# Kernel tuning notes

Hardware: AMD Instinct MI355X
Metric: run time of the kernel (lower is better)

The kernel has to match this reference:

```python
import jax, jax.numpy as jnp
import numpy as np

# BEV grid parameters from calculate_birds_eye_view_parameters([-50,50,0.5],[-50,50,0.5],[-10,10,20])
BEV_RES = np.array([0.5, 0.5, 20.0], dtype=np.float32)
BEV_START = np.array([-49.75, -49.75, 0.0], dtype=np.float32)   # lower + res/2
BEV_DIM = (200, 200, 1)                                          # (X, Y, Z)

B, N, D, H, W, C = 2, 6, 48, 28, 60, 64


def setup_inputs() -> dict:
    key = jax.random.key(0)
    k1, k2, k3 = jax.random.split(key, 3)
    x = jax.random.normal(k1, (B, N, D, H, W, C), dtype=jnp.float32)
    geo_xy = jax.random.uniform(k2, (B, N, D, H, W, 2), minval=-55.0, maxval=55.0)
    geo_z = jax.random.uniform(k3, (B, N, D, H, W, 1), minval=-12.0, maxval=12.0)
    geometry = jnp.concatenate([geo_xy, geo_z], axis=-1).astype(jnp.float32)
    return {"x": x, "geometry": geometry}


def reference(x, geometry):
    # x:        [B, N, D, H, W, C] camera frustum features
    # geometry: [B, N, D, H, W, 3] ego-frame (x, y, z) of each frustum point
    b, n, d, h, w, c = x.shape
    res = jnp.asarray(BEV_RES)
    start = jnp.asarray(BEV_START)
    dim = jnp.asarray(BEV_DIM, dtype=jnp.int32)
    X, Y, Z = BEV_DIM
    nvox = X * Y * Z

    # voxel index; torch .long() truncates toward zero -> astype(int32) matches
    vox = ((geometry - (start - res / 2.0)) / res).astype(jnp.int32)   # [B,N,D,H,W,3]
    vox = vox.reshape(b, -1, 3)                                        # [B, Np, 3]
    feat = x.reshape(b, -1, c)                                         # [B, Np, C]

    valid = jnp.all((vox >= 0) & (vox < dim), axis=-1)                 # [B, Np]
    ranks = vox[..., 0] * (Y * Z) + vox[..., 1] * Z + vox[..., 2]      # [B, Np]
    seg = jnp.where(valid, ranks + jnp.arange(b, dtype=jnp.int32)[:, None] * nvox,
                    b * nvox)                                          # invalid -> dump segment

    # per-voxel sum == sorted cumsum + dedup-diff of VoxelsSumming
    pooled = jax.ops.segment_sum(feat.reshape(-1, c), seg.reshape(-1),
                                 num_segments=b * nvox + 1)            # [B*nvox+1, C]
    bev = pooled[: b * nvox].reshape(b, X, Y, Z, c)                    # [B, X, Y, Z, C]
    # torch scatters into [Z, X, Y, C], permutes to [Z, C, X, Y], squeezes Z=1 -> [B, C, X, Y]
    out = bev.transpose(0, 3, 4, 1, 2).reshape(b, Z * c, X, Y)
    return out
```

## Files before the change

kernel.cpp:

```cpp
#include <hip/hip_runtime.h>

#define Bq 2
#define Nn 6
#define Dd 48
#define Hh 28
#define Ww 60
#define Cc 64
#define Xd 200
#define Yd 200
#define NP (Nn*Dd*Hh*Ww)
#define TOTP (Bq*NP)
#define NVOX (Xd*Yd)
#define NSEG (Bq*NVOX)
#define NB1  79

__global__ __launch_bounds__(1024) void zero_cnt(int* __restrict__ cnt)
{
    int i = blockIdx.x * 1024 + threadIdx.x;
    if (i < NSEG) cnt[i] = 0;
}

__global__ __launch_bounds__(256) void phase_a(
    const float* __restrict__ geom, int* __restrict__ rank, int* __restrict__ cnt)
{
    int p = blockIdx.x * 256 + threadIdx.x;
    if (p >= TOTP) return;
    float gx = geom[(long)p*3 + 0];
    float gy = geom[(long)p*3 + 1];
    float gz = geom[(long)p*3 + 2];
    int vx = (int)((gx + 50.0f) / 0.5f);
    int vy = (int)((gy + 50.0f) / 0.5f);
    int vz = (int)((gz + 10.0f) / 20.0f);
    int seg = -1;
    if (vx >= 0 && vx < Xd && vy >= 0 && vy < Yd && vz == 0) {
        int b = (p >= NP) ? 1 : 0;
        seg = b * NVOX + vx * Yd + vy;
        atomicAdd(&cnt[seg], 1);
    }
    rank[p] = seg;
}

__global__ __launch_bounds__(1024) void scan_p1(
    const int* __restrict__ cnt, int* __restrict__ start, int* __restrict__ bsum)
{
    __shared__ int sh[1024];
    int tid = threadIdx.x;
    int i = blockIdx.x * 1024 + tid;
    int v = (i < NSEG) ? cnt[i] : 0;
    sh[tid] = v;
    __syncthreads();
    for (int off = 1; off < 1024; off <<= 1) {
        int t = (tid >= off) ? sh[tid - off] : 0;
        __syncthreads();
        sh[tid] += t;
        __syncthreads();
    }
    if (i < NSEG) start[i] = sh[tid] - v;
    if (tid == 1023) bsum[blockIdx.x] = sh[1023];
}

__global__ __launch_bounds__(128) void scan_p2(int* __restrict__ bsum)
{
    __shared__ int sh[128];
    int tid = threadIdx.x;
    int v = (tid < NB1) ? bsum[tid] : 0;
    sh[tid] = v;
    __syncthreads();
    for (int off = 1; off < 128; off <<= 1) {
        int t = (tid >= off) ? sh[tid - off] : 0;
        __syncthreads();
        sh[tid] += t;
        __syncthreads();
    }
    if (tid < NB1) bsum[tid] = sh[tid] - v;
}

__global__ __launch_bounds__(1024) void scan_p3(
    int* __restrict__ start, const int* __restrict__ bsum)
{
    int i = blockIdx.x * 1024 + threadIdx.x;
    if (i < NSEG) start[i] += bsum[blockIdx.x];
}

__global__ __launch_bounds__(256) void phase_c(
    const int* __restrict__ rank, int* __restrict__ start, int* __restrict__ order)
{
    int p = blockIdx.x * 256 + threadIdx.x;
    if (p >= TOTP) return;
    int seg = rank[p];
    if (seg < 0) return;
    int pos = atomicAdd(&start[seg], 1);
    order[pos] = p;
}

__global__ __launch_bounds__(256) void phase_d(
    const int* __restrict__ endp, const int* __restrict__ order,
    const float* __restrict__ x, float* __restrict__ out)
{
    __shared__ float tile[32][68];
    int blk  = blockIdx.x;
    int b    = blk / (NVOX/32);
    int xy0  = (blk % (NVOX/32)) * 32;
    int wv   = threadIdx.x >> 6;
    int lane = threadIdx.x & 63;
    int seg0 = b * NVOX + xy0 + wv * 8;

    int e = 0;
    if (lane < 9) {
        int idx = seg0 - 1 + lane;
        e = (idx >= 0) ? endp[idx] : 0;
    }

    int g = lane >> 4;
    int q = (lane & 15) * 4;

    for (int v = 0; v < 8; ++v) {
        int begin = __shfl(e, v);
        int endv  = __shfl(e, v + 1);
        float4 sum = make_float4(0.f, 0.f, 0.f, 0.f);
        int t = begin + g;
        for (; t + 4 < endv; t += 8) {
            int p0 = order[t];
            int p1 = order[t + 4];
            const float4 a0 = *(const float4*)(x + (long)p0 * Cc + q);
            const float4 a1 = *(const float4*)(x + (long)p1 * Cc + q);
            sum.x += a0.x + a1.x; sum.y += a0.y + a1.y;
            sum.z += a0.z + a1.z; sum.w += a0.w + a1.w;
        }
        if (t < endv) {
            int p0 = order[t];
            const float4 a0 = *(const float4*)(x + (long)p0 * Cc + q);
            sum.x += a0.x; sum.y += a0.y; sum.z += a0.z; sum.w += a0.w;
        }
        #pragma unroll
        for (int m = 16; m <= 32; m <<= 1) {
            sum.x += __shfl_xor(sum.x, m);
            sum.y += __shfl_xor(sum.y, m);
            sum.z += __shfl_xor(sum.z, m);
            sum.w += __shfl_xor(sum.w, m);
        }
        if (g == 0) *(float4*)&tile[wv*8 + v][q] = sum;
    }
    __syncthreads();

    float* dst = out + (long)b * Cc * NVOX + xy0;
    int xy = threadIdx.x & 31;
    int c0 = threadIdx.x >> 5;
    #pragma unroll
    for (int s = 0; s < 8; ++s) {
        int c = s * 8 + c0;
        dst[(long)c * NVOX + xy] = tile[xy][c];
    }
}

__global__ __launch_bounds__(256) void fiery_scatter_direct(
    const float* __restrict__ x, const float* __restrict__ geom,
    float* __restrict__ out)
{
    int wid  = blockIdx.x * 4 + (threadIdx.x >> 6);
    int lane = threadIdx.x & 63;
    if (wid >= TOTP) return;
    long gb = (long)wid * 3;
    float gx = geom[gb+0], gy = geom[gb+1], gz = geom[gb+2];
    int vx = (int)((gx + 50.0f) / 0.5f);
    int vy = (int)((gy + 50.0f) / 0.5f);
    int vz = (int)((gz + 10.0f) / 20.0f);
    if (!(vx >= 0 && vx < Xd && vy >= 0 && vy < Yd && vz == 0)) return;
    int b = (wid >= NP) ? 1 : 0;
    float vv = x[(long)wid * Cc + lane];
    long dst = ((long)(b * Cc + lane)) * NVOX + (vx * Yd + vy);
    atomicAdd(&out[dst], vv);
}

extern "C" void kernel_launch(void* const* d_in, const int* in_sizes, int n_in,
                              void* d_out, int out_size, void* d_ws, size_t ws_size,
                              hipStream_t stream)
{
    const float* x    = (const float*)d_in[0];
    const float* geom = (const float*)d_in[1];
    float* out = (float*)d_out;

    size_t need = ((size_t)TOTP * 2 + (size_t)NSEG * 2 + 128) * sizeof(int);
    if (ws_size >= need) {
        int* rank  = (int*)d_ws;
        int* order = rank  + TOTP;
        int* cnt   = order + TOTP;
        int* start = cnt   + NSEG;
        int* bsum  = start + NSEG;

        zero_cnt<<<NB1, 1024, 0, stream>>>(cnt);
        phase_a<<<TOTP/256, 256, 0, stream>>>(geom, rank, cnt);
        scan_p1<<<NB1, 1024, 0, stream>>>(cnt, start, bsum);
        scan_p2<<<1, 128, 0, stream>>>(bsum);
        scan_p3<<<NB1, 1024, 0, stream>>>(start, bsum);
        phase_c<<<TOTP/256, 256, 0, stream>>>(rank, start, order);
        phase_d<<<Bq*(NVOX/32), 256, 0, stream>>>(start, order, x, out);
    } else {
        hipMemsetAsync(out, 0, (size_t)out_size * sizeof(float), stream);
        fiery_scatter_direct<<<TOTP/4, 256, 0, stream>>>(x, geom, out);
    }
}
```

Baseline: 130.3 us.

## Flatten per-wave voxel gather with LDS-staged indices and shared atomics

Each wave in the gather kernel now processes all points of its 8 voxels as one flat list instead of looping voxel by voxel. It first stages the point indices, tagged with their local voxel id, in shared memory, then gathers feature rows and accumulates them into the output tile with shared-memory float atomics. This is meant to remove lane idling and per-voxel shuffle reductions when voxels hold only a few points. It adds LDS atomic contention and a barrier inside a wave-divergent branch. A fallback to the per-voxel loop remains for waves whose 8 voxels hold more than 512 points.

```diff
diff --git a/kernel.cpp b/kernel.cpp
--- a/kernel.cpp
+++ b/kernel.cpp
@@ -13,6 +13,7 @@
 #define NVOX (Xd*Yd)
 #define NSEG (Bq*NVOX)
 #define NB1  79
+#define CAP  512
 
 __global__ __launch_bounds__(1024) void zero_cnt(int* __restrict__ cnt)
 {
@@ -97,6 +98,7 @@
     const int* __restrict__ endp, const int* __restrict__ order,
     const float* __restrict__ x, float* __restrict__ out)
 {
+    __shared__ int   ord_sh[4][CAP];
     __shared__ float tile[32][68];
     int blk  = blockIdx.x;
     int b    = blk / (NVOX/32);
@@ -110,36 +112,64 @@
         int idx = seg0 - 1 + lane;
         e = (idx >= 0) ? endp[idx] : 0;
     }
+    int eb0 = __shfl(e,0), eb1 = __shfl(e,1), eb2 = __shfl(e,2),
+        eb3 = __shfl(e,3), eb4 = __shfl(e,4), eb5 = __shfl(e,5),
+        eb6 = __shfl(e,6), eb7 = __shfl(e,7), eb8 = __shfl(e,8);
+    int count = eb8 - eb0;
+
+    {
+        int r = wv*8 + (lane >> 3);
+        int c = (lane & 7) * 8;
+        float4 z = make_float4(0.f, 0.f, 0.f, 0.f);
+        *(float4*)&tile[r][c]     = z;
+        *(float4*)&tile[r][c + 4] = z;
+    }
 
     int g = lane >> 4;
     int q = (lane & 15) * 4;
 
-    for (int v = 0; v < 8; ++v) {
-        int begin = __shfl(e, v);
-        int endv  = __shfl(e, v + 1);
-        float4 sum = make_float4(0.f, 0.f, 0.f, 0.f);
-        int t = begin + g;
-        for (; t + 4 < endv; t += 8) {
-            int p0 = order[t];
-            int p1 = order[t + 4];
-            const float4 a0 = *(const float4*)(x + (long)p0 * Cc + q);
-            const float4 a1 = *(const float4*)(x + (long)p1 * Cc + q);
-            sum.x += a0.x + a1.x; sum.y += a0.y + a1.y;
-            sum.z += a0.z + a1.z; sum.w += a0.w + a1.w;
+    if (count <= CAP) {
+        for (int i = lane; i < count; i += 64) {
+            int gi  = eb0 + i;
+            int pid = order[gi];
+            int v = (gi >= eb1) + (gi >= eb2) + (gi >= eb3) + (gi >= eb4)
+                  + (gi >= eb5) + (gi >= eb6) + (gi >= eb7);
+            ord_sh[wv][i] = pid | (v << 24);
         }
-        if (t < endv) {
-            int p0 = order[t];
-            const float4 a0 = *(const float4*)(x + (long)p0 * Cc + q);
-            sum.x += a0.x; sum.y += a0.y; sum.z += a0.z; sum.w += a0.w;
+        __syncthreads();
+
+        #pragma unroll 4
+        for (int i = g; i < count; i += 4) {
+            int w   = ord_sh[wv][i];
+            int pid = w & 0xFFFFFF;
+            int v   = w >> 24;
+            const float4 a = *(const float4*)(x + (long)pid * Cc + q);
+            float* row = &tile[wv*8 + v][q];
+            atomicAdd(&row[0], a.x);
+            atomicAdd(&row[1], a.y);
+            atomicAdd(&row[2], a.z);
+            atomicAdd(&row[3], a.w);
         }
-        #pragma unroll
-        for (int m = 16; m <= 32; m <<= 1) {
-            sum.x += __shfl_xor(sum.x, m);
-            sum.y += __shfl_xor(sum.y, m);
-            sum.z += __shfl_xor(sum.z, m);
-            sum.w += __shfl_xor(sum.w, m);
+    } else {
+        __syncthreads();
+        for (int v = 0; v < 8; ++v) {
+            int begin = __shfl(e, v);
+            int endv  = __shfl(e, v + 1);
+            float4 sum = make_float4(0.f, 0.f, 0.f, 0.f);
+            for (int t = begin + g; t < endv; t += 4) {
+                int p0 = order[t];
+                const float4 a0 = *(const float4*)(x + (long)p0 * Cc + q);
+                sum.x += a0.x; sum.y += a0.y; sum.z += a0.z; sum.w += a0.w;
+            }
+            #pragma unroll
+            for (int m = 16; m <= 32; m <<= 1) {
+                sum.x += __shfl_xor(sum.x, m);
+                sum.y += __shfl_xor(sum.y, m);
+                sum.z += __shfl_xor(sum.z, m);
+                sum.w += __shfl_xor(sum.w, m);
+            }
+            if (g == 0) *(float4*)&tile[wv*8 + v][q] = sum;
         }
-        if (g == 0) *(float4*)&tile[wv*8 + v][q] = sum;
     }
     __syncthreads();
 
```

After: 362.2 us. 178% more time.

## Stage gathered feature rows into LDS via async global_load_lds in pooling kernel

Applied to the files above, without the earlier changes.

The pooling kernel now stages each wave's point indices in shared memory. It then issues up to 32 row gathers per round with global_load_lds, waits on them once, and accumulates the eight voxel sums from LDS instead of chaining dependent global loads per voxel. The goal is more memory-level parallelism across all eight voxels a wave owns. In exchange it uses a large amount of LDS (about 41 KB per block), which lowers occupancy, and it adds a full vmcnt wait per round. Waves with more than 512 points fall back to a direct gather path.

```diff
diff --git a/kernel.cpp b/kernel.cpp
--- a/kernel.cpp
+++ b/kernel.cpp
@@ -13,6 +13,8 @@
 #define NVOX (Xd*Yd)
 #define NSEG (Bq*NVOX)
 #define NB1  79
+#define CAP  512
+#define RND  32
 
 __global__ __launch_bounds__(1024) void zero_cnt(int* __restrict__ cnt)
 {
@@ -93,10 +95,17 @@
     order[pos] = p;
 }
 
+#define DMA_ROW(gp, lp) \
+    __builtin_amdgcn_global_load_lds( \
+        (const __attribute__((address_space(1))) void*)(gp), \
+        (__attribute__((address_space(3))) void*)(lp), 4, 0, 0)
+
 __global__ __launch_bounds__(256) void phase_d(
     const int* __restrict__ endp, const int* __restrict__ order,
     const float* __restrict__ x, float* __restrict__ out)
 {
+    __shared__ int   ord_sh[4][CAP];
+    __shared__ float pbuf[4][RND][Cc];
     __shared__ float tile[32][68];
     int blk  = blockIdx.x;
     int b    = blk / (NVOX/32);
@@ -110,36 +119,72 @@
         int idx = seg0 - 1 + lane;
         e = (idx >= 0) ? endp[idx] : 0;
     }
+    int eb0 = __shfl(e, 0);
+    int rb[9];
+    #pragma unroll
+    for (int j = 0; j < 9; ++j) rb[j] = __shfl(e, j) - eb0;
+    int count = rb[8];
 
     int g = lane >> 4;
     int q = (lane & 15) * 4;
 
+    float4 A[8];
+    #pragma unroll
+    for (int v = 0; v < 8; ++v) A[v] = make_float4(0.f, 0.f, 0.f, 0.f);
+
+    if (count <= CAP) {
+        for (int i = lane; i < count; i += 64)
+            ord_sh[wv][i] = order[eb0 + i];
+
+        for (int base = 0; base < count; base += RND) {
+            int n = count - base; if (n > RND) n = RND;
+            int pidv = 0;
+            if (lane < RND) pidv = ord_sh[wv][base + lane];
+            #pragma unroll
+            for (int j = 0; j < RND; ++j) {
+                if (base + j < count) {
+                    int spid = __builtin_amdgcn_readlane(pidv, j);
+                    const float* gp = x + (size_t)spid * Cc + lane;
+                    DMA_ROW(gp, &pbuf[wv][j][0]);
+                }
+            }
+            asm volatile("s_waitcnt vmcnt(0)" ::: "memory");
+            #pragma unroll
+            for (int v = 0; v < 8; ++v) {
+                int lo = rb[v]   - base; if (lo < 0) lo = 0;
+                int hi = rb[v+1] - base; if (hi > n) hi = n;
+                for (int t = lo + g; t < hi; t += 4) {
+                    const float4 a = *(const float4*)&pbuf[wv][t][q];
+                    A[v].x += a.x; A[v].y += a.y;
+                    A[v].z += a.z; A[v].w += a.w;
+                }
+            }
+        }
+    } else {
+        #pragma unroll
+        for (int v = 0; v < 8; ++v) {
+            int begin = eb0 + rb[v];
+            int endv  = eb0 + rb[v+1];
+            for (int t = begin + g; t < endv; t += 4) {
+                int p0 = order[t];
+                const float4 a0 = *(const float4*)(x + (long)p0 * Cc + q);
+                A[v].x += a0.x; A[v].y += a0.y;
+                A[v].z += a0.z; A[v].w += a0.w;
+            }
+        }
+    }
+
+    #pragma unroll
     for (int v = 0; v < 8; ++v) {
-        int begin = __shfl(e, v);
-        int endv  = __shfl(e, v + 1);
-        float4 sum = make_float4(0.f, 0.f, 0.f, 0.f);
-        int t = begin + g;
-        for (; t + 4 < endv; t += 8) {
-            int p0 = order[t];
-            int p1 = order[t + 4];
-            const float4 a0 = *(const float4*)(x + (long)p0 * Cc + q);
-            const float4 a1 = *(const float4*)(x + (long)p1 * Cc + q);
-            sum.x += a0.x + a1.x; sum.y += a0.y + a1.y;
-            sum.z += a0.z + a1.z; sum.w += a0.w + a1.w;
-        }
-        if (t < endv) {
-            int p0 = order[t];
-            const float4 a0 = *(const float4*)(x + (long)p0 * Cc + q);
-            sum.x += a0.x; sum.y += a0.y; sum.z += a0.z; sum.w += a0.w;
-        }
+        A[v].x += __shfl_xor(A[v].x, 16); A[v].y += __shfl_xor(A[v].y, 16);
+        A[v].z += __shfl_xor(A[v].z, 16); A[v].w += __shfl_xor(A[v].w, 16);
+        A[v].x += __shfl_xor(A[v].x, 32); A[v].y += __shfl_xor(A[v].y, 32);
+        A[v].z += __shfl_xor(A[v].z, 32); A[v].w += __shfl_xor(A[v].w, 32);
+    }
+    if (g == 0) {
         #pragma unroll
-        for (int m = 16; m <= 32; m <<= 1) {
-            sum.x += __shfl_xor(sum.x, m);
-            sum.y += __shfl_xor(sum.y, m);
-            sum.z += __shfl_xor(sum.z, m);
-            sum.w += __shfl_xor(sum.w, m);
-        }
-        if (g == 0) *(float4*)&tile[wv*8 + v][q] = sum;
+        for (int v = 0; v < 8; ++v)
+            *(float4*)&tile[wv*8 + v][q] = A[v];
     }
     __syncthreads();
 
```

Result: slower. 134.2 us (+2.9%).

## Scatter fp16-packed feature payloads in counting-sort phase instead of index order

Applied to the files above, without the earlier changes.

The placement phase now writes each valid point's features, converted to fp16 and packed two per word, into a voxel-sorted payload buffer, replacing the index-only order array. The reduction kernel then reads these payloads contiguously per voxel instead of gathering rows of x through an indirection. This is meant to turn random gathers into coalesced streaming reads and to halve the bytes read during reduction. In exchange, it adds a full-size scattered write pass and loses precision by rounding inputs to fp16 before summing.

```diff
diff --git a/kernel.cpp b/kernel.cpp
--- a/kernel.cpp
+++ b/kernel.cpp
@@ -82,27 +82,51 @@
     if (i < NSEG) start[i] += bsum[blockIdx.x];
 }
 
-__global__ __launch_bounds__(256) void phase_c(
-    const int* __restrict__ rank, int* __restrict__ start, int* __restrict__ order)
-{
-    int p = blockIdx.x * 256 + threadIdx.x;
-    if (p >= TOTP) return;
+__global__ __launch_bounds__(256) void phase_c_pay(
+    const int* __restrict__ rank, int* __restrict__ start,
+    const float* __restrict__ x, unsigned int* __restrict__ perm)
+{
+    int w    = blockIdx.x * 4 + (threadIdx.x >> 6);
+    int lane = threadIdx.x & 63;
+    int half = lane >> 5;
+    int li   = lane & 31;
+    int p    = 2 * w + half;
+
     int seg = rank[p];
-    if (seg < 0) return;
-    int pos = atomicAdd(&start[seg], 1);
-    order[pos] = p;
-}
+    bool valid = seg >= 0;
+    int pos = 0;
+    if (li == 0 && valid) pos = atomicAdd(&start[seg], 1);
+    pos = __shfl(pos, half << 5);
+
+    if (valid) {
+        const float2 v = *(const float2*)(x + (size_t)p * Cc + 2 * li);
+        _Float16 h0 = (_Float16)v.x, h1 = (_Float16)v.y;
+        unsigned int u = (unsigned int)__builtin_bit_cast(unsigned short, h0)
+                       | ((unsigned int)__builtin_bit_cast(unsigned short, h1) << 16);
+        perm[(size_t)pos * 32 + li] = u;
+    }
+}
+
+#define VOX_LOOP(v, rA, rB) \
+    for (int r = (rA) + half; r < (rB); r += 2) { \
+        unsigned int u = base[(size_t)r * 32]; \
+        float lo = (float)__builtin_bit_cast(_Float16, (unsigned short)(u & 0xffffu)); \
+        float hi = (float)__builtin_bit_cast(_Float16, (unsigned short)(u >> 16)); \
+        Alo[v] += lo; Ahi[v] += hi; \
+    }
 
 __global__ __launch_bounds__(256) void phase_d(
-    const int* __restrict__ endp, const int* __restrict__ order,
-    const float* __restrict__ x, float* __restrict__ out)
-{
-    __shared__ float tile[32][68];
+    const int* __restrict__ endp, const unsigned int* __restrict__ perm,
+    float* __restrict__ out)
+{
+    __shared__ float tile[32][66];
     int blk  = blockIdx.x;
     int b    = blk / (NVOX/32);
     int xy0  = (blk % (NVOX/32)) * 32;
     int wv   = threadIdx.x >> 6;
     int lane = threadIdx.x & 63;
+    int half = lane >> 5;
+    int li   = lane & 31;
     int seg0 = b * NVOX + xy0 + wv * 8;
 
     int e = 0;
@@ -110,36 +134,35 @@
         int idx = seg0 - 1 + lane;
         e = (idx >= 0) ? endp[idx] : 0;
     }
-
-    int g = lane >> 4;
-    int q = (lane & 15) * 4;
-
+    int eb0 = __shfl(e, 0);
+    int rb1 = __shfl(e,1) - eb0, rb2 = __shfl(e,2) - eb0,
+        rb3 = __shfl(e,3) - eb0, rb4 = __shfl(e,4) - eb0,
+        rb5 = __shfl(e,5) - eb0, rb6 = __shfl(e,6) - eb0,
+        rb7 = __shfl(e,7) - eb0, rb8 = __shfl(e,8) - eb0;
+
+    float Alo[8], Ahi[8];
+    #pragma unroll
+    for (int v = 0; v < 8; ++v) { Alo[v] = 0.0f; Ahi[v] = 0.0f; }
+
+    const unsigned int* base = perm + (size_t)eb0 * 32 + li;
+    VOX_LOOP(0, 0,   rb1)
+    VOX_LOOP(1, rb1, rb2)
+    VOX_LOOP(2, rb2, rb3)
+    VOX_LOOP(3, rb3, rb4)
+    VOX_LOOP(4, rb4, rb5)
+    VOX_LOOP(5, rb5, rb6)
+    VOX_LOOP(6, rb6, rb7)
+    VOX_LOOP(7, rb7, rb8)
+
+    #pragma unroll
     for (int v = 0; v < 8; ++v) {
-        int begin = __shfl(e, v);
-        int endv  = __shfl(e, v + 1);
-        float4 sum = make_float4(0.f, 0.f, 0.f, 0.f);
-        int t = begin + g;
-        for (; t + 4 < endv; t += 8) {
-            int p0 = order[t];
-            int p1 = order[t + 4];
-            const float4 a0 = *(const float4*)(x + (long)p0 * Cc + q);
-            const float4 a1 = *(const float4*)(x + (long)p1 * Cc + q);
-            sum.x += a0.x + a1.x; sum.y += a0.y + a1.y;
-            sum.z += a0.z + a1.z; sum.w += a0.w + a1.w;
-        }
-        if (t < endv) {
-            int p0 = order[t];
-            const float4 a0 = *(const float4*)(x + (long)p0 * Cc + q);
-            sum.x += a0.x; sum.y += a0.y; sum.z += a0.z; sum.w += a0.w;
-        }
+        Alo[v] += __shfl_xor(Alo[v], 32);
+        Ahi[v] += __shfl_xor(Ahi[v], 32);
+    }
+    if (half == 0) {
         #pragma unroll
-        for (int m = 16; m <= 32; m <<= 1) {
-            sum.x += __shfl_xor(sum.x, m);
-            sum.y += __shfl_xor(sum.y, m);
-            sum.z += __shfl_xor(sum.z, m);
-            sum.w += __shfl_xor(sum.w, m);
-        }
-        if (g == 0) *(float4*)&tile[wv*8 + v][q] = sum;
+        for (int v = 0; v < 8; ++v)
+            *(float2*)&tile[wv*8 + v][2*li] = make_float2(Alo[v], Ahi[v]);
     }
     __syncthreads();
 
@@ -180,21 +203,22 @@
     const float* geom = (const float*)d_in[1];
     float* out = (float*)d_out;
 
-    size_t need = ((size_t)TOTP * 2 + (size_t)NSEG * 2 + 128) * sizeof(int);
+    size_t need = ((size_t)TOTP + (size_t)NSEG * 2 + 128 + (size_t)TOTP * 32)
+                  * sizeof(int);
     if (ws_size >= need) {
         int* rank  = (int*)d_ws;
-        int* order = rank  + TOTP;
-        int* cnt   = order + TOTP;
+        int* cnt   = rank  + TOTP;
         int* start = cnt   + NSEG;
         int* bsum  = start + NSEG;
+        unsigned int* perm = (unsigned int*)(bsum + 128);
 
         zero_cnt<<<NB1, 1024, 0, stream>>>(cnt);
         phase_a<<<TOTP/256, 256, 0, stream>>>(geom, rank, cnt);
         scan_p1<<<NB1, 1024, 0, stream>>>(cnt, start, bsum);
         scan_p2<<<1, 128, 0, stream>>>(bsum);
         scan_p3<<<NB1, 1024, 0, stream>>>(start, bsum);
-        phase_c<<<TOTP/256, 256, 0, stream>>>(rank, start, order);
-        phase_d<<<Bq*(NVOX/32), 256, 0, stream>>>(start, order, x, out);
+        phase_c_pay<<<TOTP/8, 256, 0, stream>>>(rank, start, x, perm);
+        phase_d<<<Bq*(NVOX/32), 256, 0, stream>>>(start, perm, out);
     } else {
         hipMemsetAsync(out, 0, (size_t)out_size * sizeof(float), stream);
         fiery_scatter_direct<<<TOTP/4, 256, 0, stream>>>(x, geom, out);
```

After: 214.1 us. 64.3% more time.
